# Kernel optimization log

Measured on AMD Instinct MI355X. Metric: run time of the kernel, lower is better.

## Reference

```python
import jax, jax.numpy as jnp
import numpy as np

NUM_USERS = 100000
NUM_ITEMS = 50000
EMBED_DIM = 64
N_LAYERS = 3
N_EDGES = 4000000
BATCH = 1024
N_NODES = NUM_USERS + NUM_ITEMS


def setup_inputs() -> dict:
    key = jax.random.key(0)
    k1, k2, k3, k4, k5, k6 = jax.random.split(key, 6)
    user_emb = jax.random.normal(k1, (NUM_USERS, EMBED_DIM), dtype=jnp.float32) * 0.1
    item_emb = jax.random.normal(k2, (NUM_ITEMS, EMBED_DIM), dtype=jnp.float32) * 0.1
    # COO representation of the symmetric-normalized adjacency (values ~ 1/sqrt(di*dj))
    edge_val = jax.random.uniform(k3, (N_EDGES,), dtype=jnp.float32)
    edge_src = jax.random.randint(k4, (N_EDGES,), 0, N_NODES, dtype=jnp.int32)
    edge_dst = jax.random.randint(k5, (N_EDGES,), 0, N_NODES, dtype=jnp.int32)
    users = jax.random.randint(k6, (BATCH,), 0, NUM_USERS, dtype=jnp.int32)
    return {
        "user_emb": user_emb,
        "item_emb": item_emb,
        "edge_val": edge_val,
        "edge_src": edge_src,
        "edge_dst": edge_dst,
        "users": users,
    }


def reference(user_emb, item_emb, edge_val, edge_src, edge_dst, users):
    # computer(): layer-wise sparse propagation with running sum (mean at the end)
    all_emb = jnp.concatenate([user_emb, item_emb], axis=0)  # [N, D]
    acc = all_emb
    emb = all_emb
    for _ in range(N_LAYERS):
        # SpMM: out[i] = sum_{(i,j) in E} val_ij * emb[j]
        msg = emb[edge_dst] * edge_val[:, None]               # [E, D] gather
        emb = jax.ops.segment_sum(msg, edge_src, num_segments=N_NODES)
        acc = acc + emb
    light_out = acc / jnp.float32(N_LAYERS + 1)               # mean over stacked layers
    all_users = light_out[:NUM_USERS]
    all_items = light_out[NUM_USERS:]
    # get_user_ratings(): batch of users scored against all items
    user_embeds = all_users[users]                            # [B, D]
    ratings = user_embeds @ all_items.T                       # [B, num_items]
    return ratings
```

## Files before the change

kernel.cpp:

```cpp
#include <hip/hip_runtime.h>
#include <hip/hip_fp16.h>

#define NUM_USERS 100000
#define NUM_ITEMS 50000
#define EMBED_DIM 64
#define N_NODES 150000
#define N_EDGES 4000000
#define N_LAYERS 3
#define BATCH 1024

#define NBKT 293
#define CHUNK 8192
#define NBLK_A ((N_EDGES + CHUNK - 1) / CHUNK)

typedef float f32x4 __attribute__((ext_vector_type(4)));

__global__ void clear_uflag_kernel(int* __restrict__ uflag) {
    int i = blockIdx.x * blockDim.x + threadIdx.x;
    if (i < NUM_USERS) uflag[i] = 0;
}

__global__ void mark_users_kernel(const int* __restrict__ users, int* __restrict__ uflag) {
    int i = blockIdx.x * blockDim.x + threadIdx.x;
    if (i < BATCH) uflag[users[i]] = 1;
}

__global__ void init_emb_kernel(const float* __restrict__ ue, const float* __restrict__ ie,
                                const int* __restrict__ uflag,
                                float* __restrict__ acc, __half2* __restrict__ h0) {
    int i = blockIdx.x * blockDim.x + threadIdx.x;
    const int total  = N_NODES * (EMBED_DIM / 4);
    const int usplit = NUM_USERS * (EMBED_DIM / 4);
    if (i < total) {
        float4 v = (i < usplit) ? reinterpret_cast<const float4*>(ue)[i]
                                : reinterpret_cast<const float4*>(ie)[i - usplit];
        h0[i * 2 + 0] = __float22half2_rn(make_float2(v.x, v.y));
        h0[i * 2 + 1] = __float22half2_rn(make_float2(v.z, v.w));
        int n = i >> 4;
        if (n >= NUM_USERS || uflag[n])
            reinterpret_cast<float4*>(acc)[i] = v;
    }
}

__global__ void histA_kernel(const int* __restrict__ src, int* __restrict__ hist) {
    __shared__ int lcnt[NBKT];
    int blk = blockIdx.x, t = threadIdx.x;
    for (int b = t; b < NBKT; b += 256) lcnt[b] = 0;
    __syncthreads();
    int e0 = blk * CHUNK;
    for (int i = t; i < CHUNK; i += 256) {
        int e = e0 + i;
        if (e < N_EDGES) atomicAdd(&lcnt[src[e] >> 9], 1);
    }
    __syncthreads();
    for (int b = t; b < NBKT; b += 256) hist[blk * NBKT + b] = lcnt[b];
}

__global__ void scanA_kernel(const int* __restrict__ hist, int* __restrict__ off,
                             int* __restrict__ bucketTotal) {
    __shared__ int arr[NBLK_A];
    int b = blockIdx.x, t = threadIdx.x;
    for (int i = t; i < NBLK_A; i += 256) arr[i] = hist[i * NBKT + b];
    __syncthreads();
    if (t == 0) {
        int run = 0;
        for (int i = 0; i < NBLK_A; ++i) { int v = arr[i]; arr[i] = run; run += v; }
        bucketTotal[b] = run;
    }
    __syncthreads();
    for (int i = t; i < NBLK_A; i += 256) off[i * NBKT + b] = arr[i];
}

__global__ void scanB_kernel(const int* __restrict__ bucketTotal, int* __restrict__ bucketBase,
                             int* __restrict__ rowptr) {
    __shared__ int s[512];
    int t = threadIdx.x;
    s[t] = (t < NBKT) ? bucketTotal[t] : 0;
    __syncthreads();
    for (int o = 1; o < 512; o <<= 1) {
        int v = (t >= o) ? s[t - o] : 0;
        __syncthreads();
        s[t] += v;
        __syncthreads();
    }
    if (t < NBKT) bucketBase[t] = (t > 0) ? s[t - 1] : 0;
    if (t == 0) { bucketBase[NBKT] = s[NBKT - 1]; rowptr[N_NODES] = N_EDGES; }
}

__global__ void partA3_kernel(const int* __restrict__ src, const int* __restrict__ dst,
                              const float* __restrict__ val, const int* __restrict__ off,
                              const int* __restrict__ bucketBase, int2* __restrict__ tmp) {
    __shared__ int lcnt[NBKT];
    int blk = blockIdx.x, t = threadIdx.x;
    for (int b = t; b < NBKT; b += 256) lcnt[b] = 0;
    __syncthreads();
    int e0 = blk * CHUNK;
    for (int i = t; i < CHUNK; i += 256) {
        int e = e0 + i;
        if (e < N_EDGES) {
            int s = src[e];
            int b = s >> 9;
            int r = atomicAdd(&lcnt[b], 1);
            int pos = bucketBase[b] + off[blk * NBKT + b] + r;
            tmp[pos] = make_int2(dst[e] | ((s & 511) << 18), __float_as_int(val[e]));
        }
    }
}

__global__ void passB_kernel(const int2* __restrict__ tmp, const int* __restrict__ bucketBase,
                             int* __restrict__ rowptr, int2* __restrict__ edge_s) {
    __shared__ int sdeg[512];
    __shared__ int cursor[512];
    int bkt = blockIdx.x;
    int t = threadIdx.x;
    int base = bucketBase[bkt];
    int cntE = bucketBase[bkt + 1] - base;
    sdeg[t] = 0;
    __syncthreads();
    for (int i = t; i < cntE; i += 512)
        atomicAdd(&sdeg[tmp[base + i].x >> 18], 1);
    __syncthreads();
    int d = sdeg[t];
    for (int o = 1; o < 512; o <<= 1) {
        int v = (t >= o) ? sdeg[t - o] : 0;
        __syncthreads();
        sdeg[t] += v;
        __syncthreads();
    }
    int excl = sdeg[t] - d;
    cursor[t] = excl;
    int n = (bkt << 9) + t;
    if (n < N_NODES) rowptr[n] = base + excl;
    __syncthreads();
    for (int i = t; i < cntE; i += 512) {
        int2 e = tmp[base + i];
        int p = base + atomicAdd(&cursor[e.x >> 18], 1);
        edge_s[p] = make_int2(e.x & 0x3FFFF, e.y);
    }
}

template <bool WRITE_NXT>
__global__ void gather_layer_kernel(const __half* __restrict__ emb, const int* __restrict__ rowptr,
                                    const int2* __restrict__ eg, const int* __restrict__ uflag,
                                    __half* __restrict__ nxt, float* __restrict__ acc) {
    int tid = blockIdx.x * 256 + threadIdx.x;
    int n = tid >> 3;
    if (n >= N_NODES) return;
    bool needed = (n >= NUM_USERS) || uflag[n];
    if (!WRITE_NXT && !needed) return;
    int c = (tid & 7) * 8;
    int beg = rowptr[n];
    int end = rowptr[n + 1];
    float a0 = 0.f, a1 = 0.f, a2 = 0.f, a3 = 0.f;
    float a4 = 0.f, a5 = 0.f, a6 = 0.f, a7 = 0.f;
    int j = beg;
    for (; j + 4 <= end; j += 4) {
        int2 e0 = eg[j];     int2 e1 = eg[j + 1];
        int2 e2 = eg[j + 2]; int2 e3 = eg[j + 3];
        uint4 r0 = *reinterpret_cast<const uint4*>(emb + (long)e0.x * EMBED_DIM + c);
        uint4 r1 = *reinterpret_cast<const uint4*>(emb + (long)e1.x * EMBED_DIM + c);
        uint4 r2 = *reinterpret_cast<const uint4*>(emb + (long)e2.x * EMBED_DIM + c);
        uint4 r3 = *reinterpret_cast<const uint4*>(emb + (long)e3.x * EMBED_DIM + c);
        float v0 = __int_as_float(e0.y), v1 = __int_as_float(e1.y);
        float v2 = __int_as_float(e2.y), v3 = __int_as_float(e3.y);
#define ACC8(R, V)                                                              \
        {                                                                       \
            const __half2* hp = reinterpret_cast<const __half2*>(&R);           \
            float2 f0 = __half22float2(hp[0]); float2 f1 = __half22float2(hp[1]);\
            float2 f2 = __half22float2(hp[2]); float2 f3 = __half22float2(hp[3]);\
            a0 += f0.x * V; a1 += f0.y * V; a2 += f1.x * V; a3 += f1.y * V;     \
            a4 += f2.x * V; a5 += f2.y * V; a6 += f3.x * V; a7 += f3.y * V;     \
        }
        ACC8(r0, v0) ACC8(r1, v1) ACC8(r2, v2) ACC8(r3, v3)
    }
    for (; j < end; ++j) {
        int2 e0 = eg[j];
        uint4 r0 = *reinterpret_cast<const uint4*>(emb + (long)e0.x * EMBED_DIM + c);
        float v0 = __int_as_float(e0.y);
        ACC8(r0, v0)
    }
#undef ACC8
    if (WRITE_NXT) {
        uint4 o;
        __half2* op = reinterpret_cast<__half2*>(&o);
        op[0] = __float22half2_rn(make_float2(a0, a1));
        op[1] = __float22half2_rn(make_float2(a2, a3));
        op[2] = __float22half2_rn(make_float2(a4, a5));
        op[3] = __float22half2_rn(make_float2(a6, a7));
        *reinterpret_cast<uint4*>(nxt + (long)n * EMBED_DIM + c) = o;
    }
    if (needed) {
        float* ap = acc + (long)n * EMBED_DIM + c;
        float4 x0 = *reinterpret_cast<float4*>(ap);
        float4 x1 = *reinterpret_cast<float4*>(ap + 4);
        x0.x += a0; x0.y += a1; x0.z += a2; x0.w += a3;
        x1.x += a4; x1.y += a5; x1.z += a6; x1.w += a7;
        *reinterpret_cast<float4*>(ap)     = x0;
        *reinterpret_cast<float4*>(ap + 4) = x1;
    }
}

#define RT_BK 32
__global__ __launch_bounds__(256, 2)
void ratings_kernel(const float* __restrict__ acc, const int* __restrict__ users,
                    float* __restrict__ out) {
    __shared__ float A[RT_BK][256 + 4];
    __shared__ float B[RT_BK][128 + 4];
    const int t  = threadIdx.x;
    const int tr = t >> 4;
    const int tc = t & 15;
    const int u0 = blockIdx.y * 256;
    const int i0 = blockIdx.x * 128;

    float cr[16][8];
#pragma unroll
    for (int a = 0; a < 16; ++a)
#pragma unroll
        for (int b = 0; b < 8; ++b) cr[a][b] = 0.f;

    for (int kk = 0; kk < EMBED_DIM; kk += RT_BK) {
        __syncthreads();
#pragma unroll
        for (int j = 0; j < 8; ++j) {
            int idx = j * 256 + t;
            int row = idx >> 3;
            int kc  = idx & 7;
            int gu  = users[u0 + row];
            float4 v = *reinterpret_cast<const float4*>(acc + (long)gu * EMBED_DIM + kk + kc * 4);
            A[kc * 4 + 0][row] = v.x; A[kc * 4 + 1][row] = v.y;
            A[kc * 4 + 2][row] = v.z; A[kc * 4 + 3][row] = v.w;
        }
#pragma unroll
        for (int j = 0; j < 4; ++j) {
            int idx = j * 256 + t;
            int row = idx >> 3;
            int kc  = idx & 7;
            int gi  = i0 + row; if (gi >= NUM_ITEMS) gi = NUM_ITEMS - 1;
            float4 v = *reinterpret_cast<const float4*>(acc + (long)(NUM_USERS + gi) * EMBED_DIM + kk + kc * 4);
            B[kc * 4 + 0][row] = v.x; B[kc * 4 + 1][row] = v.y;
            B[kc * 4 + 2][row] = v.z; B[kc * 4 + 3][row] = v.w;
        }
        __syncthreads();
#pragma unroll
        for (int k = 0; k < RT_BK; ++k) {
            float av[16];
#pragma unroll
            for (int q = 0; q < 4; ++q) {
                float4 aq = *reinterpret_cast<const float4*>(&A[k][tr * 16 + q * 4]);
                av[q * 4 + 0] = aq.x; av[q * 4 + 1] = aq.y;
                av[q * 4 + 2] = aq.z; av[q * 4 + 3] = aq.w;
            }
            float4 b0 = *reinterpret_cast<const float4*>(&B[k][tc * 4]);
            float4 b1 = *reinterpret_cast<const float4*>(&B[k][tc * 4 + 64]);
            float bv[8] = {b0.x, b0.y, b0.z, b0.w, b1.x, b1.y, b1.z, b1.w};
#pragma unroll
            for (int a = 0; a < 16; ++a)
#pragma unroll
                for (int b = 0; b < 8; ++b) cr[a][b] += av[a] * bv[b];
        }
    }

    const float inv = 1.0f / 16.0f;
#pragma unroll
    for (int uu = 0; uu < 16; ++uu) {
        long base = (long)(u0 + tr * 16 + uu) * NUM_ITEMS;
        int ia = i0 + tc * 4;
        if (ia < NUM_ITEMS) {
            f32x4 v = {cr[uu][0] * inv, cr[uu][1] * inv, cr[uu][2] * inv, cr[uu][3] * inv};
            __builtin_nontemporal_store(v, reinterpret_cast<f32x4*>(out + base + ia));
        }
        int ib = ia + 64;
        if (ib < NUM_ITEMS) {
            f32x4 v = {cr[uu][4] * inv, cr[uu][5] * inv, cr[uu][6] * inv, cr[uu][7] * inv};
            __builtin_nontemporal_store(v, reinterpret_cast<f32x4*>(out + base + ib));
        }
    }
}

extern "C" void kernel_launch(void* const* d_in, const int* in_sizes, int n_in,
                              void* d_out, int out_size, void* d_ws, size_t ws_size,
                              hipStream_t stream) {
    const float* ue    = (const float*)d_in[0];
    const float* ie    = (const float*)d_in[1];
    const float* val   = (const float*)d_in[2];
    const int*   src   = (const int*)d_in[3];
    const int*   dst   = (const int*)d_in[4];
    const int*   users = (const int*)d_in[5];
    float* out = (float*)d_out;

    const size_t tab = (size_t)N_NODES * EMBED_DIM;
    float*  acc   = (float*)d_ws;
    __half* h0    = (__half*)(acc + tab);
    __half* h1    = h0 + tab;
    int*    uflag = (int*)(h1 + tab);

    char* ob = (char*)d_out;
    int2* edge_s      = (int2*)(ob);
    int2* tmp         = (int2*)(ob + (64u << 20));
    int*  hist        = (int*) (ob + (96u << 20));
    int*  off         = (int*) (ob + (98u << 20));
    int*  bucketTotal = (int*) (ob + (100u << 20));
    int*  bucketBase  = (int*) (ob + (101u << 20));
    int*  rowptr      = (int*) (ob + (102u << 20));

    clear_uflag_kernel<<<(NUM_USERS + 255) / 256, 256, 0, stream>>>(uflag);
    mark_users_kernel<<<(BATCH + 255) / 256, 256, 0, stream>>>(users, uflag);

    const int totalv = N_NODES * EMBED_DIM / 4;
    init_emb_kernel<<<(totalv + 255) / 256, 256, 0, stream>>>(ue, ie, uflag, acc, (__half2*)h0);

    histA_kernel <<<NBLK_A, 256, 0, stream>>>(src, hist);
    scanA_kernel <<<NBKT, 256, 0, stream>>>(hist, off, bucketTotal);
    scanB_kernel <<<1, 512, 0, stream>>>(bucketTotal, bucketBase, rowptr);
    partA3_kernel<<<NBLK_A, 256, 0, stream>>>(src, dst, val, off, bucketBase, tmp);
    passB_kernel <<<NBKT, 512, 0, stream>>>(tmp, bucketBase, rowptr, edge_s);

    const int ggrid = (N_NODES * 8 + 255) / 256;
    gather_layer_kernel<true><<<ggrid, 256, 0, stream>>>(h0, rowptr, edge_s, uflag, h1, acc);
    gather_layer_kernel<true><<<ggrid, 256, 0, stream>>>(h1, rowptr, edge_s, uflag, h0, acc);
    gather_layer_kernel<false><<<ggrid, 256, 0, stream>>>(h0, rowptr, edge_s, uflag, h1, acc);

    dim3 rgrid((NUM_ITEMS + 127) / 128, BATCH / 256);
    ratings_kernel<<<rgrid, 256, 0, stream>>>(acc, users, out);
}
```

Baseline: 430.1 us.

## Use fp16 MFMA for ratings GEMM and parallelize bucket scan

Replaces the FP32 register-tiled ratings GEMM with a pack kernel that converts gathered user and item rows to fp16, followed by an MFMA 16x16x32 kernel that reads operands straight from global memory. The scanA kernel now runs a parallel Hillis-Steele scan over 512 threads instead of a serial single-thread loop. Together these aim to cut GEMM compute time and the scan's serial latency. The cost is an extra pack pass, lower precision in the dot products, and narrower, less coalesced 4-byte output stores.

```diff
diff --git a/kernel.cpp b/kernel.cpp
--- a/kernel.cpp
+++ b/kernel.cpp
@@ -14,6 +14,8 @@
 #define NBLK_A ((N_EDGES + CHUNK - 1) / CHUNK)
 
 typedef float f32x4 __attribute__((ext_vector_type(4)));
+typedef _Float16 f16x8 __attribute__((ext_vector_type(8)));
+typedef float f32x4a __attribute__((ext_vector_type(4)));
 
 __global__ void clear_uflag_kernel(int* __restrict__ uflag) {
     int i = blockIdx.x * blockDim.x + threadIdx.x;
@@ -58,17 +60,19 @@
 
 __global__ void scanA_kernel(const int* __restrict__ hist, int* __restrict__ off,
                              int* __restrict__ bucketTotal) {
-    __shared__ int arr[NBLK_A];
+    __shared__ int s[512];
     int b = blockIdx.x, t = threadIdx.x;
-    for (int i = t; i < NBLK_A; i += 256) arr[i] = hist[i * NBKT + b];
-    __syncthreads();
-    if (t == 0) {
-        int run = 0;
-        for (int i = 0; i < NBLK_A; ++i) { int v = arr[i]; arr[i] = run; run += v; }
-        bucketTotal[b] = run;
-    }
-    __syncthreads();
-    for (int i = t; i < NBLK_A; i += 256) off[i * NBKT + b] = arr[i];
+    int v0 = (t < NBLK_A) ? hist[t * NBKT + b] : 0;
+    s[t] = v0;
+    __syncthreads();
+    for (int o = 1; o < 512; o <<= 1) {
+        int v = (t >= o) ? s[t - o] : 0;
+        __syncthreads();
+        s[t] += v;
+        __syncthreads();
+    }
+    if (t < NBLK_A) off[t * NBKT + b] = s[t] - v0;
+    if (t == NBLK_A - 1) bucketTotal[b] = s[t];
 }
 
 __global__ void scanB_kernel(const int* __restrict__ bucketTotal, int* __restrict__ bucketBase,
@@ -200,81 +204,84 @@
     }
 }
 
-#define RT_BK 32
-__global__ __launch_bounds__(256, 2)
-void ratings_kernel(const float* __restrict__ acc, const int* __restrict__ users,
-                    float* __restrict__ out) {
-    __shared__ float A[RT_BK][256 + 4];
-    __shared__ float B[RT_BK][128 + 4];
-    const int t  = threadIdx.x;
-    const int tr = t >> 4;
-    const int tc = t & 15;
-    const int u0 = blockIdx.y * 256;
-    const int i0 = blockIdx.x * 128;
-
-    float cr[16][8];
+__global__ void pack_ab_kernel(const float* __restrict__ acc, const int* __restrict__ users,
+                               __half* __restrict__ A16, __half* __restrict__ B16) {
+    int tid = blockIdx.x * 256 + threadIdx.x;
+    const int total = (BATCH + NUM_ITEMS) * 8;
+    if (tid >= total) return;
+    int r = tid >> 3;
+    int c = (tid & 7) * 8;
+    const float* src;
+    __half* dstp;
+    if (r < BATCH) {
+        src  = acc + (long)users[r] * EMBED_DIM + c;
+        dstp = A16 + (long)r * EMBED_DIM + c;
+    } else {
+        int i = r - BATCH;
+        src  = acc + (long)(NUM_USERS + i) * EMBED_DIM + c;
+        dstp = B16 + (long)i * EMBED_DIM + c;
+    }
+    float4 v0 = *reinterpret_cast<const float4*>(src);
+    float4 v1 = *reinterpret_cast<const float4*>(src + 4);
+    uint4 o;
+    __half2* op = reinterpret_cast<__half2*>(&o);
+    op[0] = __float22half2_rn(make_float2(v0.x, v0.y));
+    op[1] = __float22half2_rn(make_float2(v0.z, v0.w));
+    op[2] = __float22half2_rn(make_float2(v1.x, v1.y));
+    op[3] = __float22half2_rn(make_float2(v1.z, v1.w));
+    *reinterpret_cast<uint4*>(dstp) = o;
+}
+
+__global__ __launch_bounds__(256)
+void ratings_mfma_kernel(const __half* __restrict__ A16, const __half* __restrict__ B16,
+                         float* __restrict__ out) {
+    const int w  = threadIdx.x >> 6;
+    const int l  = threadIdx.x & 63;
+    const int u0 = blockIdx.y * 32 + (w & 1) * 16;
+    const int i0 = blockIdx.x * 128 + (w >> 1) * 64;
+    const int row = l & 15;
+    const int kq  = (l >> 4) * 8;
+
+    f32x4a acc0 = {0.f, 0.f, 0.f, 0.f};
+    f32x4a acc1 = {0.f, 0.f, 0.f, 0.f};
+    f32x4a acc2 = {0.f, 0.f, 0.f, 0.f};
+    f32x4a acc3 = {0.f, 0.f, 0.f, 0.f};
+
 #pragma unroll
-    for (int a = 0; a < 16; ++a)
-#pragma unroll
-        for (int b = 0; b < 8; ++b) cr[a][b] = 0.f;
-
-    for (int kk = 0; kk < EMBED_DIM; kk += RT_BK) {
-        __syncthreads();
-#pragma unroll
-        for (int j = 0; j < 8; ++j) {
-            int idx = j * 256 + t;
-            int row = idx >> 3;
-            int kc  = idx & 7;
-            int gu  = users[u0 + row];
-            float4 v = *reinterpret_cast<const float4*>(acc + (long)gu * EMBED_DIM + kk + kc * 4);
-            A[kc * 4 + 0][row] = v.x; A[kc * 4 + 1][row] = v.y;
-            A[kc * 4 + 2][row] = v.z; A[kc * 4 + 3][row] = v.w;
-        }
-#pragma unroll
-        for (int j = 0; j < 4; ++j) {
-            int idx = j * 256 + t;
-            int row = idx >> 3;
-            int kc  = idx & 7;
-            int gi  = i0 + row; if (gi >= NUM_ITEMS) gi = NUM_ITEMS - 1;
-            float4 v = *reinterpret_cast<const float4*>(acc + (long)(NUM_USERS + gi) * EMBED_DIM + kk + kc * 4);
-            B[kc * 4 + 0][row] = v.x; B[kc * 4 + 1][row] = v.y;
-            B[kc * 4 + 2][row] = v.z; B[kc * 4 + 3][row] = v.w;
-        }
-        __syncthreads();
-#pragma unroll
-        for (int k = 0; k < RT_BK; ++k) {
-            float av[16];
-#pragma unroll
-            for (int q = 0; q < 4; ++q) {
-                float4 aq = *reinterpret_cast<const float4*>(&A[k][tr * 16 + q * 4]);
-                av[q * 4 + 0] = aq.x; av[q * 4 + 1] = aq.y;
-                av[q * 4 + 2] = aq.z; av[q * 4 + 3] = aq.w;
-            }
-            float4 b0 = *reinterpret_cast<const float4*>(&B[k][tc * 4]);
-            float4 b1 = *reinterpret_cast<const float4*>(&B[k][tc * 4 + 64]);
-            float bv[8] = {b0.x, b0.y, b0.z, b0.w, b1.x, b1.y, b1.z, b1.w};
-#pragma unroll
-            for (int a = 0; a < 16; ++a)
-#pragma unroll
-                for (int b = 0; b < 8; ++b) cr[a][b] += av[a] * bv[b];
-        }
+    for (int ks = 0; ks < EMBED_DIM; ks += 32) {
+        f16x8 a = *reinterpret_cast<const f16x8*>(A16 + (long)(u0 + row) * EMBED_DIM + ks + kq);
+        int ir0 = i0 + 0 * 16 + row; if (ir0 >= NUM_ITEMS) ir0 = NUM_ITEMS - 1;
+        int ir1 = i0 + 1 * 16 + row; if (ir1 >= NUM_ITEMS) ir1 = NUM_ITEMS - 1;
+        int ir2 = i0 + 2 * 16 + row; if (ir2 >= NUM_ITEMS) ir2 = NUM_ITEMS - 1;
+        int ir3 = i0 + 3 * 16 + row; if (ir3 >= NUM_ITEMS) ir3 = NUM_ITEMS - 1;
+        f16x8 b0 = *reinterpret_cast<const f16x8*>(B16 + (long)ir0 * EMBED_DIM + ks + kq);
+        f16x8 b1 = *reinterpret_cast<const f16x8*>(B16 + (long)ir1 * EMBED_DIM + ks + kq);
+        f16x8 b2 = *reinterpret_cast<const f16x8*>(B16 + (long)ir2 * EMBED_DIM + ks + kq);
+        f16x8 b3 = *reinterpret_cast<const f16x8*>(B16 + (long)ir3 * EMBED_DIM + ks + kq);
+        acc0 = __builtin_amdgcn_mfma_f32_16x16x32_f16(a, b0, acc0, 0, 0, 0);
+        acc1 = __builtin_amdgcn_mfma_f32_16x16x32_f16(a, b1, acc1, 0, 0, 0);
+        acc2 = __builtin_amdgcn_mfma_f32_16x16x32_f16(a, b2, acc2, 0, 0, 0);
+        acc3 = __builtin_amdgcn_mfma_f32_16x16x32_f16(a, b3, acc3, 0, 0, 0);
     }
 
     const float inv = 1.0f / 16.0f;
-#pragma unroll
-    for (int uu = 0; uu < 16; ++uu) {
-        long base = (long)(u0 + tr * 16 + uu) * NUM_ITEMS;
-        int ia = i0 + tc * 4;
-        if (ia < NUM_ITEMS) {
-            f32x4 v = {cr[uu][0] * inv, cr[uu][1] * inv, cr[uu][2] * inv, cr[uu][3] * inv};
-            __builtin_nontemporal_store(v, reinterpret_cast<f32x4*>(out + base + ia));
-        }
-        int ib = ia + 64;
-        if (ib < NUM_ITEMS) {
-            f32x4 v = {cr[uu][4] * inv, cr[uu][5] * inv, cr[uu][6] * inv, cr[uu][7] * inv};
-            __builtin_nontemporal_store(v, reinterpret_cast<f32x4*>(out + base + ib));
-        }
-    }
+    const int orow = u0 + (l >> 4) * 4;
+    const int colb = l & 15;
+#define STORE_FRAG(ACC, C)                                                      \
+    {                                                                           \
+        int col = i0 + (C) * 16 + colb;                                         \
+        if (col < NUM_ITEMS) {                                                  \
+            __builtin_nontemporal_store(ACC[0] * inv, out + (long)(orow + 0) * NUM_ITEMS + col); \
+            __builtin_nontemporal_store(ACC[1] * inv, out + (long)(orow + 1) * NUM_ITEMS + col); \
+            __builtin_nontemporal_store(ACC[2] * inv, out + (long)(orow + 2) * NUM_ITEMS + col); \
+            __builtin_nontemporal_store(ACC[3] * inv, out + (long)(orow + 3) * NUM_ITEMS + col); \
+        }                                                                       \
+    }
+    STORE_FRAG(acc0, 0)
+    STORE_FRAG(acc1, 1)
+    STORE_FRAG(acc2, 2)
+    STORE_FRAG(acc3, 3)
+#undef STORE_FRAG
 }
 
 extern "C" void kernel_launch(void* const* d_in, const int* in_sizes, int n_in,
@@ -294,6 +301,9 @@
     __half* h1    = h0 + tab;
     int*    uflag = (int*)(h1 + tab);
 
+    __half* A16 = h1;
+    __half* B16 = h1 + (size_t)BATCH * EMBED_DIM;
+
     char* ob = (char*)d_out;
     int2* edge_s      = (int2*)(ob);
     int2* tmp         = (int2*)(ob + (64u << 20));
@@ -310,7 +320,7 @@
     init_emb_kernel<<<(totalv + 255) / 256, 256, 0, stream>>>(ue, ie, uflag, acc, (__half2*)h0);
 
     histA_kernel <<<NBLK_A, 256, 0, stream>>>(src, hist);
-    scanA_kernel <<<NBKT, 256, 0, stream>>>(hist, off, bucketTotal);
+    scanA_kernel <<<NBKT, 512, 0, stream>>>(hist, off, bucketTotal);
     scanB_kernel <<<1, 512, 0, stream>>>(bucketTotal, bucketBase, rowptr);
     partA3_kernel<<<NBLK_A, 256, 0, stream>>>(src, dst, val, off, bucketBase, tmp);
     passB_kernel <<<NBKT, 512, 0, stream>>>(tmp, bucketBase, rowptr, edge_s);
@@ -320,6 +330,9 @@
     gather_layer_kernel<true><<<ggrid, 256, 0, stream>>>(h1, rowptr, edge_s, uflag, h0, acc);
     gather_layer_kernel<false><<<ggrid, 256, 0, stream>>>(h0, rowptr, edge_s, uflag, h1, acc);
 
-    dim3 rgrid((NUM_ITEMS + 127) / 128, BATCH / 256);
-    ratings_kernel<<<rgrid, 256, 0, stream>>>(acc, users, out);
-}
+    const int packn = (BATCH + NUM_ITEMS) * 8;
+    pack_ab_kernel<<<(packn + 255) / 256, 256, 0, stream>>>(acc, users, A16, B16);
+
+    dim3 rgrid((NUM_ITEMS + 127) / 128, BATCH / 32);
+    ratings_mfma_kernel<<<rgrid, 256, 0, stream>>>(A16, B16, out);
+}
```

Result: faster. 389.4 us (-9.5%).
